# Optimization experiments

Measured on AMD Instinct MI355X. Metric: run time of the kernel, lower is better.

Reference implementation:

```python
import jax, jax.numpy as jnp
import numpy as np

N = 50000      # nodes
E = 800000     # edges
D_IN = 128
D_H = 128
D_OUT = 64


def _glorot(key, fan_in, fan_out):
    s = float(np.sqrt(6.0 / (fan_in + fan_out)))
    return jax.random.uniform(key, (fan_in, fan_out), jnp.float32, -s, s)


def setup_inputs() -> dict:
    key = jax.random.key(0)
    ks = jax.random.split(key, 8)
    x = jax.random.normal(ks[0], (N, D_IN), jnp.float32)
    edge_index = jax.random.randint(ks[1], (2, E), 0, N, dtype=jnp.int32)
    return {
        "x": x,
        "edge_index": edge_index,
        "W0": _glorot(ks[2], D_IN, D_H), "b0": jnp.zeros((D_H,), jnp.float32),
        "W1": _glorot(ks[3], D_H, D_H),  "b1": jnp.zeros((D_H,), jnp.float32),
        "W2": _glorot(ks[4], D_H, D_H),  "b2": jnp.zeros((D_H,), jnp.float32),
        "W_out": _glorot(ks[5], D_H, D_OUT), "b_out": jnp.zeros((D_OUT,), jnp.float32),
    }


def reference(x, edge_index, W0, b0, W1, b1, W2, b2, W_out, b_out):
    src = edge_index[0]
    dst = edge_index[1]
    # GCN normalization with self-loops: deg = in-degree(dst) + 1
    deg = jax.ops.segment_sum(jnp.ones((E,), x.dtype), dst, num_segments=N) + 1.0
    dinv = jax.lax.rsqrt(deg)                       # [N]
    edge_coef = (dinv[src] * dinv[dst])[:, None]    # [E,1]
    self_coef = (dinv * dinv)[:, None]              # [N,1]

    def gcn_conv(h, W, b):
        h = h @ W                                            # [N,F]
        agg = jax.ops.segment_sum(h[src] * edge_coef, dst, num_segments=N)
        agg = agg + h * self_coef                            # self-loop term
        return agg + b

    h = x
    for W, b in ((W0, b0), (W1, b1), (W2, b2)):
        h_in = h
        h = jax.nn.relu(gcn_conv(h, W, b))  # eval mode: dropout is identity
        if h.shape == h_in.shape:
            h = h + h_in
    return h @ W_out + b_out
```

## Files before the change

### kernel.cpp

```cpp
#include <hip/hip_runtime.h>

#define N_NODES 50000
#define N_EDGES 800000

static inline int cdiv(int a, int b) { return (a + b - 1) / b; }

typedef __attribute__((ext_vector_type(8))) short s8vec;
typedef __attribute__((ext_vector_type(4))) float f32x4;

__device__ inline ushort f2b(float f) {
    uint u = __float_as_uint(f);
    uint r = (u + 0x7fffu + ((u >> 16) & 1u)) >> 16;
    return (ushort)r;
}
__device__ inline float b2f_lo(uint v) { return __uint_as_float(v << 16); }
__device__ inline float b2f_hi(uint v) { return __uint_as_float(v & 0xffff0000u); }

__device__ inline void add8(float* acc, uint4 v) {
    acc[0] += b2f_lo(v.x); acc[1] += b2f_hi(v.x);
    acc[2] += b2f_lo(v.y); acc[3] += b2f_hi(v.y);
    acc[4] += b2f_lo(v.z); acc[5] += b2f_hi(v.z);
    acc[6] += b2f_lo(v.w); acc[7] += b2f_hi(v.w);
}


__global__ __launch_bounds__(256) void k_prep(int* cnt,
                                              const float* __restrict__ W0, const float* __restrict__ W1,
                                              const float* __restrict__ W2, const float* __restrict__ Wo,
                                              ushort* Wt0, ushort* Wt1, ushort* Wt2, ushort* Wto) {
    int b = blockIdx.x;
    if (b < 196) {
        int i = b * 256 + threadIdx.x;
        if (i < N_NODES) cnt[i] = 0;
        return;
    }
    int i = (b - 196) * 256 + threadIdx.x;
    if (i < 16384) {
        int nn = i >> 7, k = i & 127;
        Wt0[i] = f2b(W0[k * 128 + nn]);
    } else if (i < 32768) {
        int j = i - 16384; int nn = j >> 7, k = j & 127;
        Wt1[j] = f2b(W1[k * 128 + nn]);
    } else if (i < 49152) {
        int j = i - 32768; int nn = j >> 7, k = j & 127;
        Wt2[j] = f2b(W2[k * 128 + nn]);
    } else if (i < 57344) {
        int j = i - 49152; int nn = j >> 7, k = j & 127;
        Wto[j] = f2b(Wo[k * 64 + nn]);
    }
}

__global__ __launch_bounds__(256) void k_count(const int* __restrict__ dst, int* cnt, int e) {
    int i = blockIdx.x * 256 + threadIdx.x;
    if (i < e) atomicAdd(&cnt[dst[i]], 1);
}


__global__ __launch_bounds__(512) void k_block_sum(const int* __restrict__ cnt, int* bsum, int n) {
    __shared__ int sh[512];
    int i = blockIdx.x * 512 + threadIdx.x;
    sh[threadIdx.x] = (i < n) ? cnt[i] : 0;
    __syncthreads();
    for (int off = 256; off > 0; off >>= 1) {
        if (threadIdx.x < off) sh[threadIdx.x] += sh[threadIdx.x + off];
        __syncthreads();
    }
    if (threadIdx.x == 0) bsum[blockIdx.x] = sh[0];
}

__global__ __launch_bounds__(128) void k_scan_bsum(const int* __restrict__ bsum, int* boff,
                                                   int nb, int* rowptr, int n, int e) {
    __shared__ int sh[128];
    int t = threadIdx.x;
    int v = (t < nb) ? bsum[t] : 0;
    sh[t] = v;
    __syncthreads();
    for (int off = 1; off < 128; off <<= 1) {
        int add = (t >= off) ? sh[t - off] : 0;
        __syncthreads();
        sh[t] += add;
        __syncthreads();
    }
    if (t < nb) boff[t] = sh[t] - v;
    if (t == 0) rowptr[n] = e;
}

__global__ __launch_bounds__(512) void k_scan_block(const int* __restrict__ cnt,
                                                    const int* __restrict__ boff,
                                                    int* rowptr, int* cursor, float* dinv, int n) {
    __shared__ int sh[512];
    int t = threadIdx.x;
    int i = blockIdx.x * 512 + t;
    int v = (i < n) ? cnt[i] : 0;
    sh[t] = v;
    __syncthreads();
    for (int off = 1; off < 512; off <<= 1) {
        int add = (t >= off) ? sh[t - off] : 0;
        __syncthreads();
        sh[t] += add;
        __syncthreads();
    }
    if (i < n) {
        int rp = sh[t] - v + boff[blockIdx.x];
        rowptr[i] = rp;
        cursor[i] = rp;
        dinv[i] = rsqrtf((float)v + 1.0f);
    }
}


template <int NCOL, bool IN_F32, bool OUT_F32, bool SCALE>
__device__ inline void mm_body(const void* __restrict__ Av, const ushort* __restrict__ Wt,
                               const float* __restrict__ bias, const float* __restrict__ dinv,
                               void* __restrict__ Cv, int n, int bid) {
    constexpr int NT = NCOL / 16;
    int wave = threadIdx.x >> 6;
    int lane = threadIdx.x & 63;
    int quad = lane >> 4;
    int lm = lane & 15;
    int row0 = bid * 128 + wave * 32;

    int rA0 = row0 + lm;      if (rA0 > n - 1) rA0 = n - 1;
    int rA1 = row0 + 16 + lm; if (rA1 > n - 1) rA1 = n - 1;

    f32x4 acc[2][NT];
#pragma unroll
    for (int r = 0; r < 2; r++)
#pragma unroll
        for (int t = 0; t < NT; t++) acc[r][t] = (f32x4){0.f, 0.f, 0.f, 0.f};

    for (int kc = 0; kc < 128; kc += 32) {
        s8vec af[2];
        if (IN_F32) {
            const float* A = (const float*)Av;
#pragma unroll
            for (int r = 0; r < 2; r++) {
                const float* p = A + (size_t)(r ? rA1 : rA0) * 128 + quad * 8 + kc;
                float4 a = *(const float4*)p, b = *(const float4*)(p + 4);
                s8vec v;
                v[0] = (short)f2b(a.x); v[1] = (short)f2b(a.y);
                v[2] = (short)f2b(a.z); v[3] = (short)f2b(a.w);
                v[4] = (short)f2b(b.x); v[5] = (short)f2b(b.y);
                v[6] = (short)f2b(b.z); v[7] = (short)f2b(b.w);
                af[r] = v;
            }
        } else {
            const ushort* A = (const ushort*)Av;
            af[0] = *(const s8vec*)(A + (size_t)rA0 * 128 + quad * 8 + kc);
            af[1] = *(const s8vec*)(A + (size_t)rA1 * 128 + quad * 8 + kc);
        }
#pragma unroll
        for (int t = 0; t < NT; t++) {
            s8vec bf = *(const s8vec*)(Wt + (size_t)(t * 16 + lm) * 128 + kc + quad * 8);
            acc[0][t] = __builtin_amdgcn_mfma_f32_16x16x32_bf16(af[0], bf, acc[0][t], 0, 0, 0);
            acc[1][t] = __builtin_amdgcn_mfma_f32_16x16x32_bf16(af[1], bf, acc[1][t], 0, 0, 0);
        }
    }

#pragma unroll
    for (int r = 0; r < 2; r++) {
#pragma unroll
        for (int i = 0; i < 4; i++) {
            int rr = row0 + r * 16 + quad * 4 + i;
            if (rr < n) {
                float dv = SCALE ? dinv[rr] : 1.0f;
#pragma unroll
                for (int t = 0; t < NT; t++) {
                    int col = t * 16 + lm;
                    if (OUT_F32)
                        ((float*)Cv)[(size_t)rr * NCOL + col] = acc[r][t][i] + bias[col];
                    else
                        ((ushort*)Cv)[(size_t)rr * 128 + col] =
                            f2b(SCALE ? acc[r][t][i] * dv : acc[r][t][i]);
                }
            }
        }
    }
}

template <int NCOL, bool IN_F32, bool OUT_F32, bool SCALE>
__global__ __launch_bounds__(256) void k_mm(const void* __restrict__ Av,
                                            const ushort* __restrict__ Wt,
                                            const float* __restrict__ bias,
                                            const float* __restrict__ dinv,
                                            void* __restrict__ Cv, int n) {
    mm_body<NCOL, IN_F32, OUT_F32, SCALE>(Av, Wt, bias, dinv, Cv, n, blockIdx.x);
}

__global__ __launch_bounds__(256) void k_mm0_fill(const void* __restrict__ Av,
                                                  const ushort* __restrict__ Wt,
                                                  const float* __restrict__ dinv,
                                                  void* __restrict__ Cv, int n, int mmblocks,
                                                  const int* __restrict__ src, const int* __restrict__ dst,
                                                  int* cursor, uint* ed, int e) {
    if ((int)blockIdx.x >= mmblocks) {
        int base = ((int)blockIdx.x - mmblocks) * 1024 + threadIdx.x;
#pragma unroll
        for (int k = 0; k < 4; k++) {
            int i = base + k * 256;
            if (i < e) {
                int d = dst[i], s = src[i];
                int pos = atomicAdd(&cursor[d], 1);
                ed[pos] = (uint)s;
            }
        }
        return;
    }
    mm_body<128, true, false, true>(Av, Wt, nullptr, dinv, Cv, n, blockIdx.x);
}


template <bool RES_F32>
__global__ __launch_bounds__(256) void k_gatherb(const uint4* __restrict__ T4,
                                                 const int* __restrict__ rowptr,
                                                 const uint* __restrict__ ed,
                                                 const float* __restrict__ dinv,
                                                 const float* __restrict__ bias,
                                                 const void* __restrict__ resv,
                                                 uint4* __restrict__ out4, int n) {
    int node = blockIdx.x * 16 + (threadIdx.x >> 4);
    if (node >= n) return;
    int ql = threadIdx.x & 15;
    int qb = threadIdx.x & 48;

    float acc[8] = {0.f, 0.f, 0.f, 0.f, 0.f, 0.f, 0.f, 0.f};
    int beg = rowptr[node], end = rowptr[node + 1];

    for (int base = beg; base < end; base += 16) {
        int m = end - base; if (m > 16) m = 16;
        int idx = base + ql; if (idx > end - 1) idx = end - 1;
        uint em = ed[idx];
        int j = 0;
        for (; j + 4 <= m; j += 4) {
            int s0 = __shfl((int)em, qb + j);
            int s1 = __shfl((int)em, qb + j + 1);
            int s2 = __shfl((int)em, qb + j + 2);
            int s3 = __shfl((int)em, qb + j + 3);
            uint4 v0 = T4[(size_t)s0 * 16 + ql];
            uint4 v1 = T4[(size_t)s1 * 16 + ql];
            uint4 v2 = T4[(size_t)s2 * 16 + ql];
            uint4 v3 = T4[(size_t)s3 * 16 + ql];
            add8(acc, v0); add8(acc, v1); add8(acc, v2); add8(acc, v3);
        }
        for (; j < m; j++) {
            int s = __shfl((int)em, qb + j);
            uint4 v = T4[(size_t)s * 16 + ql];
            add8(acc, v);
        }
    }

    uint4 vs = T4[(size_t)node * 16 + ql];
    add8(acc, vs);

    float di = dinv[node];
    float4 bv0 = ((const float4*)bias)[ql * 2];
    float4 bv1 = ((const float4*)bias)[ql * 2 + 1];
    float bb[8] = {bv0.x, bv0.y, bv0.z, bv0.w, bv1.x, bv1.y, bv1.z, bv1.w};

    float r[8];
    if (RES_F32) {
        float4 r0 = ((const float4*)resv)[(size_t)node * 32 + ql * 2];
        float4 r1 = ((const float4*)resv)[(size_t)node * 32 + ql * 2 + 1];
        r[0] = r0.x; r[1] = r0.y; r[2] = r0.z; r[3] = r0.w;
        r[4] = r1.x; r[5] = r1.y; r[6] = r1.z; r[7] = r1.w;
    } else {
        uint4 rv = ((const uint4*)resv)[(size_t)node * 16 + ql];
        r[0] = b2f_lo(rv.x); r[1] = b2f_hi(rv.x); r[2] = b2f_lo(rv.y); r[3] = b2f_hi(rv.y);
        r[4] = b2f_lo(rv.z); r[5] = b2f_hi(rv.z); r[6] = b2f_lo(rv.w); r[7] = b2f_hi(rv.w);
    }

    float o[8];
#pragma unroll
    for (int i = 0; i < 8; i++)
        o[i] = fmaxf(acc[i] * di + bb[i], 0.f) + r[i];

    uint4 ov;
    ov.x = (uint)f2b(o[0]) | ((uint)f2b(o[1]) << 16);
    ov.y = (uint)f2b(o[2]) | ((uint)f2b(o[3]) << 16);
    ov.z = (uint)f2b(o[4]) | ((uint)f2b(o[5]) << 16);
    ov.w = (uint)f2b(o[6]) | ((uint)f2b(o[7]) << 16);
    out4[(size_t)node * 16 + ql] = ov;
}


extern "C" void kernel_launch(void* const* d_in, const int* in_sizes, int n_in,
                              void* d_out, int out_size, void* d_ws, size_t ws_size,
                              hipStream_t stream) {
    const float* x  = (const float*)d_in[0];
    const int* eidx = (const int*)d_in[1];
    const float* W0 = (const float*)d_in[2];
    const float* b0 = (const float*)d_in[3];
    const float* W1 = (const float*)d_in[4];
    const float* b1 = (const float*)d_in[5];
    const float* W2 = (const float*)d_in[6];
    const float* b2 = (const float*)d_in[7];
    const float* Wo = (const float*)d_in[8];
    const float* bo = (const float*)d_in[9];
    float* out = (float*)d_out;

    const int N = N_NODES, E = N_EDGES;
    const int* srcI = eidx;
    const int* dstI = eidx + E;
    const int NB512 = cdiv(N, 512);

    char* ws = (char*)d_ws;
    auto alloc = [&](size_t bytes) { char* p = ws; ws += (bytes + 255) / 256 * 256; return p; };
    int*    cnt    = (int*)alloc((size_t)N * 4);
    int*    cursor = (int*)alloc((size_t)N * 4);
    int*    rowptr = (int*)alloc((size_t)(N + 1) * 4);
    int*    bsum   = (int*)alloc((size_t)NB512 * 4);
    int*    boff   = (int*)alloc((size_t)NB512 * 4);
    float*  dinv   = (float*)alloc((size_t)N * 4);
    uint*   ed     = (uint*)alloc((size_t)E * 4);
    ushort* tmpb   = (ushort*)alloc((size_t)N * 128 * 2);
    ushort* hAb    = (ushort*)alloc((size_t)N * 128 * 2);
    ushort* hBb    = (ushort*)alloc((size_t)N * 128 * 2);
    ushort* Wt0    = (ushort*)alloc(128 * 128 * 2);
    ushort* Wt1    = (ushort*)alloc(128 * 128 * 2);
    ushort* Wt2    = (ushort*)alloc(128 * 128 * 2);
    ushort* Wto    = (ushort*)alloc(64 * 128 * 2);

    dim3 b256(256), b512(512);

    const int mmGrid   = cdiv(N, 128);
    const int fillGrid = cdiv(E, 1024);
    const int gGrid    = cdiv(N, 16);

    k_prep<<<196 + 224, b256, 0, stream>>>(cnt, W0, W1, W2, Wo, Wt0, Wt1, Wt2, Wto);
    k_count<<<cdiv(E, 256), b256, 0, stream>>>(dstI, cnt, E);
    k_block_sum<<<NB512, b512, 0, stream>>>(cnt, bsum, N);
    k_scan_bsum<<<1, 128, 0, stream>>>(bsum, boff, NB512, rowptr, N, E);
    k_scan_block<<<NB512, b512, 0, stream>>>(cnt, boff, rowptr, cursor, dinv, N);

    k_mm0_fill<<<mmGrid + fillGrid, b256, 0, stream>>>(x, Wt0, dinv, tmpb, N, mmGrid,
                                                       srcI, dstI, cursor, ed, E);
    k_gatherb<true><<<gGrid, b256, 0, stream>>>((const uint4*)tmpb, rowptr, ed, dinv, b0, x, (uint4*)hAb, N);

    k_mm<128, false, false, true><<<mmGrid, b256, 0, stream>>>(hAb, Wt1, nullptr, dinv, tmpb, N);
    k_gatherb<false><<<gGrid, b256, 0, stream>>>((const uint4*)tmpb, rowptr, ed, dinv, b1, hAb, (uint4*)hBb, N);

    k_mm<128, false, false, true><<<mmGrid, b256, 0, stream>>>(hBb, Wt2, nullptr, dinv, tmpb, N);
    k_gatherb<false><<<gGrid, b256, 0, stream>>>((const uint4*)tmpb, rowptr, ed, dinv, b2, hBb, (uint4*)hAb, N);

    k_mm<64, false, true, false><<<mmGrid, b256, 0, stream>>>(hAb, Wto, bo, dinv, out, N);
}
```

Baseline: 308.9 us.

## Two-pass bucketed CSR fill, single-kernel scan, and 8-wide gather unroll

Merges the three scan kernels into one, where each block redundantly sums all preceding counts to get its base offset and also records per-bucket cursors. The edge scatter becomes two passes: first edges are partitioned into 512-node dst buckets using shared-memory histograms, then a second kernel scatters within buckets so that cursor atomics and ed writes hit more localized memory. The gather loop also gains an 8-edge unrolled path for more memory-level parallelism. The cost is an extra 6.4MB pairs buffer pass, an additional launch, and O(N) redundant reads in the scan.

```diff
diff --git a/kernel.cpp b/kernel.cpp
--- a/kernel.cpp
+++ b/kernel.cpp
@@ -2,6 +2,7 @@
 
 #define N_NODES 50000
 #define N_EDGES 800000
+#define NBUCKET 98
 
 static inline int cdiv(int a, int b) { return (a + b - 1) / b; }
 
@@ -56,41 +57,25 @@
 }
 
 
-__global__ __launch_bounds__(512) void k_block_sum(const int* __restrict__ cnt, int* bsum, int n) {
+__global__ __launch_bounds__(512) void k_scan_all(const int* __restrict__ cnt,
+                                                  int* rowptr, int* cursor, float* dinv,
+                                                  int* bcur, int n, int e, int nb) {
     __shared__ int sh[512];
-    int i = blockIdx.x * 512 + threadIdx.x;
-    sh[threadIdx.x] = (i < n) ? cnt[i] : 0;
+    int t = threadIdx.x, b = blockIdx.x;
+    int start = b * 512;
+
+    int partial = 0;
+    for (int i = t; i < start; i += 512) partial += cnt[i];
+    sh[t] = partial;
     __syncthreads();
     for (int off = 256; off > 0; off >>= 1) {
-        if (threadIdx.x < off) sh[threadIdx.x] += sh[threadIdx.x + off];
-        __syncthreads();
-    }
-    if (threadIdx.x == 0) bsum[blockIdx.x] = sh[0];
-}
-
-__global__ __launch_bounds__(128) void k_scan_bsum(const int* __restrict__ bsum, int* boff,
-                                                   int nb, int* rowptr, int n, int e) {
-    __shared__ int sh[128];
-    int t = threadIdx.x;
-    int v = (t < nb) ? bsum[t] : 0;
-    sh[t] = v;
+        if (t < off) sh[t] += sh[t + off];
+        __syncthreads();
+    }
+    int base = sh[0];
     __syncthreads();
-    for (int off = 1; off < 128; off <<= 1) {
-        int add = (t >= off) ? sh[t - off] : 0;
-        __syncthreads();
-        sh[t] += add;
-        __syncthreads();
-    }
-    if (t < nb) boff[t] = sh[t] - v;
-    if (t == 0) rowptr[n] = e;
-}
-
-__global__ __launch_bounds__(512) void k_scan_block(const int* __restrict__ cnt,
-                                                    const int* __restrict__ boff,
-                                                    int* rowptr, int* cursor, float* dinv, int n) {
-    __shared__ int sh[512];
-    int t = threadIdx.x;
-    int i = blockIdx.x * 512 + t;
+
+    int i = start + t;
     int v = (i < n) ? cnt[i] : 0;
     sh[t] = v;
     __syncthreads();
@@ -101,11 +86,13 @@
         __syncthreads();
     }
     if (i < n) {
-        int rp = sh[t] - v + boff[blockIdx.x];
+        int rp = base + sh[t] - v;
         rowptr[i] = rp;
         cursor[i] = rp;
         dinv[i] = rsqrtf((float)v + 1.0f);
     }
+    if (t == 0) bcur[b] = base;
+    if (b == nb - 1 && t == 0) rowptr[n] = e;
 }
 
 
@@ -187,26 +174,56 @@
     mm_body<NCOL, IN_F32, OUT_F32, SCALE>(Av, Wt, bias, dinv, Cv, n, blockIdx.x);
 }
 
-__global__ __launch_bounds__(256) void k_mm0_fill(const void* __restrict__ Av,
-                                                  const ushort* __restrict__ Wt,
-                                                  const float* __restrict__ dinv,
-                                                  void* __restrict__ Cv, int n, int mmblocks,
-                                                  const int* __restrict__ src, const int* __restrict__ dst,
-                                                  int* cursor, uint* ed, int e) {
+__global__ __launch_bounds__(256) void k_mm0_fillA(const void* __restrict__ Av,
+                                                   const ushort* __restrict__ Wt,
+                                                   const float* __restrict__ dinv,
+                                                   void* __restrict__ Cv, int n, int mmblocks,
+                                                   const int* __restrict__ src, const int* __restrict__ dst,
+                                                   int* bcur, uint2* pairs, int e) {
+    __shared__ int hist[NBUCKET], gb[NBUCKET];
     if ((int)blockIdx.x >= mmblocks) {
-        int base = ((int)blockIdx.x - mmblocks) * 1024 + threadIdx.x;
-#pragma unroll
-        for (int k = 0; k < 4; k++) {
-            int i = base + k * 256;
+        int e0 = ((int)blockIdx.x - mmblocks) * 2048;
+        if (threadIdx.x < NBUCKET) hist[threadIdx.x] = 0;
+        __syncthreads();
+        int sarr[8], darr[8], offr[8];
+#pragma unroll
+        for (int k = 0; k < 8; k++) {
+            int i = e0 + k * 256 + threadIdx.x;
+            int s = 0, d = 0, o = -1;
             if (i < e) {
-                int d = dst[i], s = src[i];
-                int pos = atomicAdd(&cursor[d], 1);
-                ed[pos] = (uint)s;
+                s = src[i]; d = dst[i];
+                o = atomicAdd(&hist[d >> 9], 1);
             }
+            sarr[k] = s; darr[k] = d; offr[k] = o;
+        }
+        __syncthreads();
+        if (threadIdx.x < NBUCKET)
+            gb[threadIdx.x] = atomicAdd(&bcur[threadIdx.x], hist[threadIdx.x]);
+        __syncthreads();
+#pragma unroll
+        for (int k = 0; k < 8; k++) {
+            if (offr[k] >= 0) {
+                int pos = gb[darr[k] >> 9] + offr[k];
+                pairs[pos] = make_uint2((uint)sarr[k], (uint)darr[k]);
+            }
         }
         return;
     }
     mm_body<128, true, false, true>(Av, Wt, nullptr, dinv, Cv, n, blockIdx.x);
+}
+
+__global__ __launch_bounds__(256) void k_fillB(const uint2* __restrict__ pairs,
+                                               int* cursor, uint* ed, int e) {
+    int i0 = blockIdx.x * 2048 + threadIdx.x;
+#pragma unroll
+    for (int k = 0; k < 8; k++) {
+        int i = i0 + k * 256;
+        if (i < e) {
+            uint2 p = pairs[i];
+            int pos = atomicAdd(&cursor[p.y], 1);
+            ed[pos] = p.x;
+        }
+    }
 }
 
 
@@ -231,6 +248,26 @@
         int idx = base + ql; if (idx > end - 1) idx = end - 1;
         uint em = ed[idx];
         int j = 0;
+        for (; j + 8 <= m; j += 8) {
+            int s0 = __shfl((int)em, qb + j);
+            int s1 = __shfl((int)em, qb + j + 1);
+            int s2 = __shfl((int)em, qb + j + 2);
+            int s3 = __shfl((int)em, qb + j + 3);
+            int s4 = __shfl((int)em, qb + j + 4);
+            int s5 = __shfl((int)em, qb + j + 5);
+            int s6 = __shfl((int)em, qb + j + 6);
+            int s7 = __shfl((int)em, qb + j + 7);
+            uint4 v0 = T4[(size_t)s0 * 16 + ql];
+            uint4 v1 = T4[(size_t)s1 * 16 + ql];
+            uint4 v2 = T4[(size_t)s2 * 16 + ql];
+            uint4 v3 = T4[(size_t)s3 * 16 + ql];
+            uint4 v4 = T4[(size_t)s4 * 16 + ql];
+            uint4 v5 = T4[(size_t)s5 * 16 + ql];
+            uint4 v6 = T4[(size_t)s6 * 16 + ql];
+            uint4 v7 = T4[(size_t)s7 * 16 + ql];
+            add8(acc, v0); add8(acc, v1); add8(acc, v2); add8(acc, v3);
+            add8(acc, v4); add8(acc, v5); add8(acc, v6); add8(acc, v7);
+        }
         for (; j + 4 <= m; j += 4) {
             int s0 = __shfl((int)em, qb + j);
             int s1 = __shfl((int)em, qb + j + 1);
@@ -301,17 +338,16 @@
     const int N = N_NODES, E = N_EDGES;
     const int* srcI = eidx;
     const int* dstI = eidx + E;
-    const int NB512 = cdiv(N, 512);
 
     char* ws = (char*)d_ws;
     auto alloc = [&](size_t bytes) { char* p = ws; ws += (bytes + 255) / 256 * 256; return p; };
     int*    cnt    = (int*)alloc((size_t)N * 4);
     int*    cursor = (int*)alloc((size_t)N * 4);
     int*    rowptr = (int*)alloc((size_t)(N + 1) * 4);
-    int*    bsum   = (int*)alloc((size_t)NB512 * 4);
-    int*    boff   = (int*)alloc((size_t)NB512 * 4);
+    int*    bcur   = (int*)alloc((size_t)NBUCKET * 4);
     float*  dinv   = (float*)alloc((size_t)N * 4);
     uint*   ed     = (uint*)alloc((size_t)E * 4);
+    uint2*  pairs  = (uint2*)alloc((size_t)E * 8);
     ushort* tmpb   = (ushort*)alloc((size_t)N * 128 * 2);
     ushort* hAb    = (ushort*)alloc((size_t)N * 128 * 2);
     ushort* hBb    = (ushort*)alloc((size_t)N * 128 * 2);
@@ -323,17 +359,16 @@
     dim3 b256(256), b512(512);
 
     const int mmGrid   = cdiv(N, 128);
-    const int fillGrid = cdiv(E, 1024);
+    const int fillGrid = cdiv(E, 2048);
     const int gGrid    = cdiv(N, 16);
 
     k_prep<<<196 + 224, b256, 0, stream>>>(cnt, W0, W1, W2, Wo, Wt0, Wt1, Wt2, Wto);
     k_count<<<cdiv(E, 256), b256, 0, stream>>>(dstI, cnt, E);
-    k_block_sum<<<NB512, b512, 0, stream>>>(cnt, bsum, N);
-    k_scan_bsum<<<1, 128, 0, stream>>>(bsum, boff, NB512, rowptr, N, E);
-    k_scan_block<<<NB512, b512, 0, stream>>>(cnt, boff, rowptr, cursor, dinv, N);
-
-    k_mm0_fill<<<mmGrid + fillGrid, b256, 0, stream>>>(x, Wt0, dinv, tmpb, N, mmGrid,
-                                                       srcI, dstI, cursor, ed, E);
+    k_scan_all<<<NBUCKET, b512, 0, stream>>>(cnt, rowptr, cursor, dinv, bcur, N, E, NBUCKET);
+
+    k_mm0_fillA<<<mmGrid + fillGrid, b256, 0, stream>>>(x, Wt0, dinv, tmpb, N, mmGrid,
+                                                        srcI, dstI, bcur, pairs, E);
+    k_fillB<<<fillGrid, b256, 0, stream>>>(pairs, cursor, ed, E);
     k_gatherb<true><<<gGrid, b256, 0, stream>>>((const uint4*)tmpb, rowptr, ed, dinv, b0, x, (uint4*)hAb, N);
 
     k_mm<128, false, false, true><<<mmGrid, b256, 0, stream>>>(hAb, Wt1, nullptr, dinv, tmpb, N);
```

Result: slower. 322.9 us (+4.5%).
